# Kernel optimization log

Hardware: AMD Instinct MI355X
Metric: run time of the kernel (lower is better)

## Reference

```python
import jax, jax.numpy as jnp
import numpy as np

N_NODES = 50000
N_EDGES = 1_600_000
IN_DIM = 128
HID = 64


def gcn_conv(x, src, dst, w, W, b, n):
    # PyG GCNConv(normalize=True, add_self_loops=True):
    # add self loops with weight 1, sym-normalize, x@W (no bias in lin), scatter-add, +bias
    loop = jnp.arange(n)
    s = jnp.concatenate([src, loop])
    d = jnp.concatenate([dst, loop])
    ww = jnp.concatenate([w, jnp.ones((n,), w.dtype)])
    deg = jax.ops.segment_sum(ww, d, num_segments=n)                 # [n]
    dis = jnp.where(deg > 0, jax.lax.rsqrt(deg), 0.0)                # deg^{-1/2}, inf->0
    norm = dis[s] * ww * dis[d]                                      # [E+n]
    h = x @ W                                                        # [n, out]
    msg = h[s] * norm[:, None]                                       # gather + scale
    out = jax.ops.segment_sum(msg, d, num_segments=n)                # scatter-add at dst
    return out + b


def setup_inputs() -> dict:
    key = jax.random.key(0)
    ks = jax.random.split(key, 9)
    X = jax.random.normal(ks[0], (N_NODES, IN_DIM), dtype=jnp.float32)
    edge_index = jax.random.randint(ks[1], (2, N_EDGES), 0, N_NODES, dtype=jnp.int64)
    edge_weight = jax.random.uniform(ks[2], (N_EDGES,), dtype=jnp.float32)
    s1 = 1.0 / np.sqrt(IN_DIM)
    s2 = 1.0 / np.sqrt(HID)
    W1 = jax.random.uniform(ks[3], (IN_DIM, HID), jnp.float32, -s1, s1)
    b1 = jax.random.uniform(ks[4], (HID,), jnp.float32, -s1, s1)
    W2 = jax.random.uniform(ks[5], (HID, HID), jnp.float32, -s2, s2)
    b2 = jax.random.uniform(ks[6], (HID,), jnp.float32, -s2, s2)
    Wl = jax.random.uniform(ks[7], (HID, 1), jnp.float32, -s2, s2)
    bl = jax.random.uniform(ks[8], (1,), jnp.float32, -s2, s2)
    return {"X": X, "edge_index": edge_index, "edge_weight": edge_weight,
            "W1": W1, "b1": b1, "W2": W2, "b2": b2, "Wl": Wl, "bl": bl}


def reference(X, edge_index, edge_weight, W1, b1, W2, b2, Wl, bl):
    n = X.shape[0]
    src, dst = edge_index[0], edge_index[1]
    h = jax.nn.relu(gcn_conv(X, src, dst, edge_weight, W1, b1, n))
    # F.dropout(p=0.2) is identity in eval mode
    h = jax.nn.relu(gcn_conv(h, src, dst, edge_weight, W2, b2, n))
    return jax.nn.sigmoid(h @ Wl + bl).squeeze(1)   # [n]
```

## Files before the change

### kernel.cpp

```cpp
#include <hip/hip_runtime.h>

typedef float f32x2 __attribute__((ext_vector_type(2)));

#define A2B 512
#define A2T 512
#define STG 3200

__device__ __forceinline__ long ld_idx(const void* idx, long pos, int is64) {
  return is64 ? (long)((const long long*)idx)[pos]
              : (long)((const int*)idx)[pos];
}

__device__ __forceinline__ int detect_is64(const void* idx) {
  const unsigned long long* p = (const unsigned long long*)idx;
  unsigned long long v = p[threadIdx.x & 63];
  return (__ballot((v >> 32) != 0ull) == 0ull) ? 1 : 0;
}

__global__ __launch_bounds__(256) void k_hist256(const void* __restrict__ idx,
                                                 unsigned* __restrict__ histT,
                                                 long E, int chunk, unsigned M) {
  __shared__ unsigned cnt[256];
  const int b = blockIdx.x, t = threadIdx.x;
  const int is64 = detect_is64(idx);
  cnt[t] = 0;
  __syncthreads();
  const long e0 = (long)b * chunk;
  long e1 = e0 + chunk; if (e1 > E) e1 = E;
  for (long e = e0 + t; e < e1; e += 256) {
    unsigned d = (unsigned)ld_idx(idx, E + e, is64);
    atomicAdd(&cnt[__umulhi(d, M)], 1u);
  }
  __syncthreads();
  histT[(size_t)t * A2B + b] = cnt[t];
}

__global__ __launch_bounds__(256) void k_colscan(const unsigned* __restrict__ histT,
                                                 unsigned* __restrict__ baseT,
                                                 unsigned* __restrict__ colsum) {
  __shared__ unsigned sh[256];
  const int k = blockIdx.x, t = threadIdx.x;
  const uint2 v = ((const uint2*)(histT + (size_t)k * A2B))[t];
  unsigned s = v.x + v.y;
  sh[t] = s;
  __syncthreads();
  for (int off = 1; off < 256; off <<= 1) {
    unsigned u = (t >= off) ? sh[t - off] : 0;
    __syncthreads();
    sh[t] += u;
    __syncthreads();
  }
  unsigned excl = sh[t] - s;
  uint2 o; o.x = excl; o.y = excl + v.x;
  ((uint2*)(baseT + (size_t)k * A2B))[t] = o;
  if (t == 255) colsum[k] = sh[255];
}

__global__ __launch_bounds__(A2T) void k_bucket(const void* __restrict__ idx,
                                                const float* __restrict__ w,
                                                const unsigned* __restrict__ baseT,
                                                const unsigned* __restrict__ colsum,
                                                uint2* __restrict__ recs,
                                                long E, int chunk, unsigned M) {
  __shared__ uint2 stage[STG];
  __shared__ unsigned cnt[256], lofs[256], lbase[256], bcol[256], scanb[256];
  const int b = blockIdx.x, t = threadIdx.x;
  const long e0 = (long)b * chunk;
  long e1 = e0 + chunk; if (e1 > E) e1 = E;
  const int m = (int)(e1 - e0);
  const int is64 = detect_is64(idx);
  if (t < 256) scanb[t] = colsum[t];
  __syncthreads();
  for (int off = 1; off < 256; off <<= 1) {
    unsigned u = 0;
    if (t < 256 && t >= off) u = scanb[t - off];
    __syncthreads();
    if (t < 256) scanb[t] += u;
    __syncthreads();
  }
  if (t < 256) {
    bcol[t] = (scanb[t] - colsum[t]) + baseT[(size_t)t * A2B + b];
    cnt[t] = 0;
  }
  __syncthreads();
  unsigned short dc[8]; unsigned char kc[8];
  int nk = 0;
  for (long e = e0 + t; e < e1; e += A2T, ++nk) {
    unsigned d = (unsigned)ld_idx(idx, E + e, is64);
    unsigned kb = __umulhi(d, M);
    dc[nk] = (unsigned short)d; kc[nk] = (unsigned char)kb;
    atomicAdd(&cnt[kb], 1u);
  }
  __syncthreads();
  if (t < 256) scanb[t] = cnt[t];
  __syncthreads();
  for (int off = 1; off < 256; off <<= 1) {
    unsigned u = 0;
    if (t < 256 && t >= off) u = scanb[t - off];
    __syncthreads();
    if (t < 256) scanb[t] += u;
    __syncthreads();
  }
  if (t < 256) { unsigned ex = scanb[t] - cnt[t]; lbase[t] = ex; lofs[t] = ex; }
  __syncthreads();
  nk = 0;
  for (long e = e0 + t; e < e1; e += A2T, ++nk) {
    unsigned s = (unsigned)ld_idx(idx, e, is64);
    float wv = w[e];
    unsigned kb = kc[nk];
    unsigned pos = atomicAdd(&lofs[kb], 1u);
    stage[pos] = make_uint2(s | ((unsigned)dc[nk] << 16), __float_as_uint(wv));
  }
  __syncthreads();
  for (int i = t; i < m; i += A2T) {
    uint2 r = stage[i];
    unsigned kb = __umulhi(r.x >> 16, M);
    recs[bcol[kb] + (unsigned)i - lbase[kb]] = r;
  }
}

__global__ __launch_bounds__(1024) void k_build(const uint2* __restrict__ recs,
                                                const unsigned* __restrict__ colsum,
                                                int* __restrict__ rowptr,
                                                float* __restrict__ dis,
                                                float2* __restrict__ edges,
                                                int n, int dwidth, long E) {
  __shared__ float wsum[256];
  __shared__ unsigned cnt[256], lofs[256], scanb[256];
  __shared__ int shr0, shr1;
  const int k = blockIdx.x, t = threadIdx.x;
  const int d0 = k * dwidth;
  if (t < 256) scanb[t] = colsum[t];
  __syncthreads();
  for (int off = 1; off < 256; off <<= 1) {
    unsigned u = 0;
    if (t < 256 && t >= off) u = scanb[t - off];
    __syncthreads();
    if (t < 256) scanb[t] += u;
    __syncthreads();
  }
  if (t == k) { shr1 = (int)scanb[t]; shr0 = (int)(scanb[t] - colsum[t]); }
  if (t < 256) { wsum[t] = 0.0f; cnt[t] = 0; }
  __syncthreads();
  const int r0 = shr0, r1 = shr1;
  const int m = r1 - r0;
  for (int i = t; i < m; i += 1024) {
    uint2 r = recs[r0 + i];
    int dl = (int)(r.x >> 16) - d0;
    atomicAdd(&cnt[dl], 1u);
    atomicAdd(&wsum[dl], __uint_as_float(r.y));
  }
  __syncthreads();
  if (t < 256) scanb[t] = cnt[t];
  __syncthreads();
  for (int off = 1; off < 256; off <<= 1) {
    unsigned u = 0;
    if (t < 256 && t >= off) u = scanb[t - off];
    __syncthreads();
    if (t < 256) scanb[t] += u;
    __syncthreads();
  }
  if (t < 256) {
    unsigned ex = scanb[t] - cnt[t];
    lofs[t] = (unsigned)r0 + ex;
    int d = d0 + t;
    if (t < dwidth && d < n) {
      rowptr[d] = r0 + (int)ex;
      dis[d] = rsqrtf(1.0f + wsum[t]);
    }
  }
  if (k == gridDim.x - 1 && t == 0) rowptr[n] = (int)E;
  __syncthreads();
  for (int i = t; i < m; i += 1024) {
    uint2 r = recs[r0 + i];
    unsigned pos = atomicAdd(&lofs[(int)(r.x >> 16) - d0], 1u);
    edges[pos] = make_float2(__uint_as_float(r.x & 0xffffu), __uint_as_float(r.y));
  }
}

__device__ __forceinline__ uint4 pack16_fp8(const float* acc) {
  uint4 o;
  unsigned v;
  v = 0;
  v = __builtin_amdgcn_cvt_pk_fp8_f32(acc[0],  acc[1],  v, false);
  v = __builtin_amdgcn_cvt_pk_fp8_f32(acc[2],  acc[3],  v, true);
  o.x = v; v = 0;
  v = __builtin_amdgcn_cvt_pk_fp8_f32(acc[4],  acc[5],  v, false);
  v = __builtin_amdgcn_cvt_pk_fp8_f32(acc[6],  acc[7],  v, true);
  o.y = v; v = 0;
  v = __builtin_amdgcn_cvt_pk_fp8_f32(acc[8],  acc[9],  v, false);
  v = __builtin_amdgcn_cvt_pk_fp8_f32(acc[10], acc[11], v, true);
  o.z = v; v = 0;
  v = __builtin_amdgcn_cvt_pk_fp8_f32(acc[12], acc[13], v, false);
  v = __builtin_amdgcn_cvt_pk_fp8_f32(acc[14], acc[15], v, true);
  o.w = v;
  return o;
}

__global__ __launch_bounds__(256) void k_gemm1(const float* __restrict__ X,
                                               const float* __restrict__ W,
                                               unsigned char* __restrict__ h, int n) {
  __shared__ float Ws[128 * 64];
  for (int i = threadIdx.x; i < 2048; i += 256)
    ((float4*)Ws)[i] = ((const float4*)W)[i];
  __syncthreads();
  int gid = blockIdx.x * 256 + threadIdx.x;
  int node = gid >> 2;
  int fg = (gid & 3) * 16;
  if (node >= n) return;
  const float4* xr4 = (const float4*)(X + (size_t)node * 128);
  float acc[16];
#pragma unroll
  for (int f = 0; f < 16; ++f) acc[f] = 0.0f;
  for (int k4 = 0; k4 < 32; ++k4) {
    float4 x = xr4[k4];
#pragma unroll
    for (int kk = 0; kk < 4; ++kk) {
      float xv = (kk == 0) ? x.x : (kk == 1) ? x.y : (kk == 2) ? x.z : x.w;
      const float4* wrow = (const float4*)(Ws + (k4 * 4 + kk) * 64 + fg);
#pragma unroll
      for (int f4 = 0; f4 < 4; ++f4) {
        float4 w = wrow[f4];
        acc[f4 * 4 + 0] = fmaf(xv, w.x, acc[f4 * 4 + 0]);
        acc[f4 * 4 + 1] = fmaf(xv, w.y, acc[f4 * 4 + 1]);
        acc[f4 * 4 + 2] = fmaf(xv, w.z, acc[f4 * 4 + 2]);
        acc[f4 * 4 + 3] = fmaf(xv, w.w, acc[f4 * 4 + 3]);
      }
    }
  }
  *(uint4*)(h + (size_t)node * 64 + fg) = pack16_fp8(acc);
}

__global__ __launch_bounds__(256) void k_gemm2(const float* __restrict__ in,
                                               const float* __restrict__ W,
                                               unsigned char* __restrict__ h, int n) {
  __shared__ float Ws[64 * 64];
  for (int i = threadIdx.x; i < 1024; i += 256)
    ((float4*)Ws)[i] = ((const float4*)W)[i];
  __syncthreads();
  int gid = blockIdx.x * 256 + threadIdx.x;
  int node = gid >> 2;
  int fg = (gid & 3) * 16;
  if (node >= n) return;
  const float4* xr4 = (const float4*)(in + (size_t)node * 64);
  float acc[16];
#pragma unroll
  for (int f = 0; f < 16; ++f) acc[f] = 0.0f;
  for (int k4 = 0; k4 < 16; ++k4) {
    float4 x = xr4[k4];
#pragma unroll
    for (int kk = 0; kk < 4; ++kk) {
      float xv = (kk == 0) ? x.x : (kk == 1) ? x.y : (kk == 2) ? x.z : x.w;
      xv = fmaxf(xv, 0.0f);
      const float4* wrow = (const float4*)(Ws + (k4 * 4 + kk) * 64 + fg);
#pragma unroll
      for (int f4 = 0; f4 < 4; ++f4) {
        float4 w = wrow[f4];
        acc[f4 * 4 + 0] = fmaf(xv, w.x, acc[f4 * 4 + 0]);
        acc[f4 * 4 + 1] = fmaf(xv, w.y, acc[f4 * 4 + 1]);
        acc[f4 * 4 + 2] = fmaf(xv, w.z, acc[f4 * 4 + 2]);
        acc[f4 * 4 + 3] = fmaf(xv, w.w, acc[f4 * 4 + 3]);
      }
    }
  }
  *(uint4*)(h + (size_t)node * 64 + fg) = pack16_fp8(acc);
}

template <int MODE>
__global__ __launch_bounds__(256) void k_gather(const unsigned char* __restrict__ h,
                                                const float* __restrict__ dis,
                                                const float2* __restrict__ edges,
                                                const int* __restrict__ rowptr,
                                                const float* __restrict__ b,
                                                const float* __restrict__ Wl,
                                                const float* __restrict__ bl,
                                                float* __restrict__ out, int n) {
  int lane = threadIdx.x & 63;
  int half = lane >> 5;
  int l32 = lane & 31;
  int fl = lane & 7;
  int eg = (lane >> 3) & 3;
  int node = blockIdx.x * 8 + (int)(threadIdx.x >> 6) * 2 + half;
  if (node >= n) return;
  int beg = rowptr[node], end = rowptr[node + 1];
  float s0 = dis[node];
  float acc[8];
#pragma unroll
  for (int i = 0; i < 8; ++i) acc[i] = 0.0f;

  for (int base = beg; base < end; base += 32) {
    int m = end - base; if (m > 32) m = 32;
    float2 pk = (l32 < m) ? edges[base + l32] : make_float2(__int_as_float(0), 0.0f);
    float nrm = dis[__float_as_int(pk.x)] * pk.y * s0;
    int steps = (m + 3) >> 2;
    for (int s = 0; s < steps; ++s) {
      int j = half * 32 + s * 4 + eg;
      int   sj = __float_as_int(__shfl(pk.x, j));
      float nj = __shfl(nrm, j);
      uint2 hv = *(const uint2*)(h + (size_t)sj * 64 + fl * 8);
      f32x2 p0 = __builtin_amdgcn_cvt_pk_f32_fp8(hv.x, false);
      f32x2 p1 = __builtin_amdgcn_cvt_pk_f32_fp8(hv.x, true);
      f32x2 p2 = __builtin_amdgcn_cvt_pk_f32_fp8(hv.y, false);
      f32x2 p3 = __builtin_amdgcn_cvt_pk_f32_fp8(hv.y, true);
      acc[0] = fmaf(p0[0], nj, acc[0]);
      acc[1] = fmaf(p0[1], nj, acc[1]);
      acc[2] = fmaf(p1[0], nj, acc[2]);
      acc[3] = fmaf(p1[1], nj, acc[3]);
      acc[4] = fmaf(p2[0], nj, acc[4]);
      acc[5] = fmaf(p2[1], nj, acc[5]);
      acc[6] = fmaf(p3[0], nj, acc[6]);
      acc[7] = fmaf(p3[1], nj, acc[7]);
    }
  }
#pragma unroll
  for (int off = 8; off < 32; off <<= 1)
#pragma unroll
    for (int i = 0; i < 8; ++i) acc[i] += __shfl_xor(acc[i], off);

  uint2 hv = *(const uint2*)(h + (size_t)node * 64 + fl * 8);
  f32x2 q0 = __builtin_amdgcn_cvt_pk_f32_fp8(hv.x, false);
  f32x2 q1 = __builtin_amdgcn_cvt_pk_f32_fp8(hv.x, true);
  f32x2 q2 = __builtin_amdgcn_cvt_pk_f32_fp8(hv.y, false);
  f32x2 q3 = __builtin_amdgcn_cvt_pk_f32_fp8(hv.y, true);
  float hs[8] = {q0[0], q0[1], q1[0], q1[1], q2[0], q2[1], q3[0], q3[1]};
  float4 bv0 = *(const float4*)(b + fl * 8);
  float4 bv1 = *(const float4*)(b + fl * 8 + 4);
  float bb[8] = {bv0.x, bv0.y, bv0.z, bv0.w, bv1.x, bv1.y, bv1.z, bv1.w};
  float s2 = s0 * s0;
#pragma unroll
  for (int i = 0; i < 8; ++i) acc[i] += bb[i] + hs[i] * s2;

  if (MODE == 0) {
    if (eg == 0) {
      float4 o0 = make_float4(acc[0], acc[1], acc[2], acc[3]);
      float4 o1 = make_float4(acc[4], acc[5], acc[6], acc[7]);
      *(float4*)(out + (size_t)node * 64 + fl * 8) = o0;
      *(float4*)(out + (size_t)node * 64 + fl * 8 + 4) = o1;
    }
  } else {
    float4 wl0 = *(const float4*)(Wl + fl * 8);
    float4 wl1 = *(const float4*)(Wl + fl * 8 + 4);
    float wl[8] = {wl0.x, wl0.y, wl0.z, wl0.w, wl1.x, wl1.y, wl1.z, wl1.w};
    float v = 0.0f;
#pragma unroll
    for (int i = 0; i < 8; ++i) v += fmaxf(acc[i], 0.0f) * wl[i];
#pragma unroll
    for (int off = 1; off < 8; off <<= 1) v += __shfl_xor(v, off);
    if (l32 == 0) out[node] = 1.0f / (1.0f + expf(-(v + bl[0])));
  }
}

extern "C" void kernel_launch(void* const* d_in, const int* in_sizes, int n_in,
                              void* d_out, int out_size, void* d_ws, size_t ws_size,
                              hipStream_t stream) {
  const float* X  = (const float*)d_in[0];
  const void*  EI = d_in[1];
  const float* EW = (const float*)d_in[2];
  const float* W1 = (const float*)d_in[3];
  const float* b1 = (const float*)d_in[4];
  const float* W2 = (const float*)d_in[5];
  const float* b2 = (const float*)d_in[6];
  const float* Wl = (const float*)d_in[7];
  const float* bl = (const float*)d_in[8];
  float* out = (float*)d_out;

  const int  n = in_sizes[0] / 128;
  const long E = (long)in_sizes[1] / 2;

  const int chunk  = (int)((E + A2B - 1) / A2B);
  const int dwidth = (n + 255) / 256;
  const unsigned M = (unsigned)((0x100000000ULL + (unsigned)dwidth - 1) / (unsigned)dwidth);

  auto align = [](size_t x) { return (x + 255) & ~(size_t)255; };
  char* ws = (char*)d_ws;
  size_t off = 0;
  float*         dis    = (float*)(ws + off);         off += align((size_t)n * 4);
  int*           rowptr = (int*)(ws + off);           off += align((size_t)(n + 1) * 4);
  unsigned*      colsum = (unsigned*)(ws + off);      off += align(256 * 4);
  unsigned*      histT  = (unsigned*)(ws + off);      off += align((size_t)A2B * 256 * 4);
  unsigned*      baseT  = (unsigned*)(ws + off);      off += align((size_t)A2B * 256 * 4);
  uint2*         recs   = (uint2*)(ws + off);         off += align((size_t)E * 8);
  float2*        edges  = (float2*)(ws + off);        off += align((size_t)E * 8);
  unsigned char* A      = (unsigned char*)(ws + off); off += align((size_t)n * 64);
  float*         B      = (float*)(ws + off);         off += align((size_t)n * 64 * 4);

  const int nbW = (n + 7) / 8;
  const int nbG = (n * 4 + 255) / 256;

  k_hist256<<<A2B, 256, 0, stream>>>(EI, histT, E, chunk, M);
  k_colscan<<<256, 256, 0, stream>>>(histT, baseT, colsum);
  k_bucket<<<A2B, A2T, 0, stream>>>(EI, EW, baseT, colsum, recs, E, chunk, M);
  k_build<<<256, 1024, 0, stream>>>(recs, colsum, rowptr, dis, edges, n, dwidth, E);

  k_gemm1<<<nbG, dim3(256), 0, stream>>>(X, W1, A, n);
  k_gather<0><<<nbW, dim3(256), 0, stream>>>(A, dis, edges, rowptr, b1, Wl, bl, B, n);

  k_gemm2<<<nbG, dim3(256), 0, stream>>>(B, W2, A, n);
  k_gather<1><<<nbW, dim3(256), 0, stream>>>(A, dis, edges, rowptr, b2, Wl, bl, out, n);
}
```

Measured before the change: 218.8 us.

## Fuse layer-1 aggregation with second GEMM and merge histogram with first GEMM

```diff
diff --git a/kernel.cpp b/kernel.cpp
--- a/kernel.cpp
+++ b/kernel.cpp
@@ -15,167 +15,6 @@
   const unsigned long long* p = (const unsigned long long*)idx;
   unsigned long long v = p[threadIdx.x & 63];
   return (__ballot((v >> 32) != 0ull) == 0ull) ? 1 : 0;
-}
-
-__global__ __launch_bounds__(256) void k_hist256(const void* __restrict__ idx,
-                                                 unsigned* __restrict__ histT,
-                                                 long E, int chunk, unsigned M) {
-  __shared__ unsigned cnt[256];
-  const int b = blockIdx.x, t = threadIdx.x;
-  const int is64 = detect_is64(idx);
-  cnt[t] = 0;
-  __syncthreads();
-  const long e0 = (long)b * chunk;
-  long e1 = e0 + chunk; if (e1 > E) e1 = E;
-  for (long e = e0 + t; e < e1; e += 256) {
-    unsigned d = (unsigned)ld_idx(idx, E + e, is64);
-    atomicAdd(&cnt[__umulhi(d, M)], 1u);
-  }
-  __syncthreads();
-  histT[(size_t)t * A2B + b] = cnt[t];
-}
-
-__global__ __launch_bounds__(256) void k_colscan(const unsigned* __restrict__ histT,
-                                                 unsigned* __restrict__ baseT,
-                                                 unsigned* __restrict__ colsum) {
-  __shared__ unsigned sh[256];
-  const int k = blockIdx.x, t = threadIdx.x;
-  const uint2 v = ((const uint2*)(histT + (size_t)k * A2B))[t];
-  unsigned s = v.x + v.y;
-  sh[t] = s;
-  __syncthreads();
-  for (int off = 1; off < 256; off <<= 1) {
-    unsigned u = (t >= off) ? sh[t - off] : 0;
-    __syncthreads();
-    sh[t] += u;
-    __syncthreads();
-  }
-  unsigned excl = sh[t] - s;
-  uint2 o; o.x = excl; o.y = excl + v.x;
-  ((uint2*)(baseT + (size_t)k * A2B))[t] = o;
-  if (t == 255) colsum[k] = sh[255];
-}
-
-__global__ __launch_bounds__(A2T) void k_bucket(const void* __restrict__ idx,
-                                                const float* __restrict__ w,
-                                                const unsigned* __restrict__ baseT,
-                                                const unsigned* __restrict__ colsum,
-                                                uint2* __restrict__ recs,
-                                                long E, int chunk, unsigned M) {
-  __shared__ uint2 stage[STG];
-  __shared__ unsigned cnt[256], lofs[256], lbase[256], bcol[256], scanb[256];
-  const int b = blockIdx.x, t = threadIdx.x;
-  const long e0 = (long)b * chunk;
-  long e1 = e0 + chunk; if (e1 > E) e1 = E;
-  const int m = (int)(e1 - e0);
-  const int is64 = detect_is64(idx);
-  if (t < 256) scanb[t] = colsum[t];
-  __syncthreads();
-  for (int off = 1; off < 256; off <<= 1) {
-    unsigned u = 0;
-    if (t < 256 && t >= off) u = scanb[t - off];
-    __syncthreads();
-    if (t < 256) scanb[t] += u;
-    __syncthreads();
-  }
-  if (t < 256) {
-    bcol[t] = (scanb[t] - colsum[t]) + baseT[(size_t)t * A2B + b];
-    cnt[t] = 0;
-  }
-  __syncthreads();
-  unsigned short dc[8]; unsigned char kc[8];
-  int nk = 0;
-  for (long e = e0 + t; e < e1; e += A2T, ++nk) {
-    unsigned d = (unsigned)ld_idx(idx, E + e, is64);
-    unsigned kb = __umulhi(d, M);
-    dc[nk] = (unsigned short)d; kc[nk] = (unsigned char)kb;
-    atomicAdd(&cnt[kb], 1u);
-  }
-  __syncthreads();
-  if (t < 256) scanb[t] = cnt[t];
-  __syncthreads();
-  for (int off = 1; off < 256; off <<= 1) {
-    unsigned u = 0;
-    if (t < 256 && t >= off) u = scanb[t - off];
-    __syncthreads();
-    if (t < 256) scanb[t] += u;
-    __syncthreads();
-  }
-  if (t < 256) { unsigned ex = scanb[t] - cnt[t]; lbase[t] = ex; lofs[t] = ex; }
-  __syncthreads();
-  nk = 0;
-  for (long e = e0 + t; e < e1; e += A2T, ++nk) {
-    unsigned s = (unsigned)ld_idx(idx, e, is64);
-    float wv = w[e];
-    unsigned kb = kc[nk];
-    unsigned pos = atomicAdd(&lofs[kb], 1u);
-    stage[pos] = make_uint2(s | ((unsigned)dc[nk] << 16), __float_as_uint(wv));
-  }
-  __syncthreads();
-  for (int i = t; i < m; i += A2T) {
-    uint2 r = stage[i];
-    unsigned kb = __umulhi(r.x >> 16, M);
-    recs[bcol[kb] + (unsigned)i - lbase[kb]] = r;
-  }
-}
-
-__global__ __launch_bounds__(1024) void k_build(const uint2* __restrict__ recs,
-                                                const unsigned* __restrict__ colsum,
-                                                int* __restrict__ rowptr,
-                                                float* __restrict__ dis,
-                                                float2* __restrict__ edges,
-                                                int n, int dwidth, long E) {
-  __shared__ float wsum[256];
-  __shared__ unsigned cnt[256], lofs[256], scanb[256];
-  __shared__ int shr0, shr1;
-  const int k = blockIdx.x, t = threadIdx.x;
-  const int d0 = k * dwidth;
-  if (t < 256) scanb[t] = colsum[t];
-  __syncthreads();
-  for (int off = 1; off < 256; off <<= 1) {
-    unsigned u = 0;
-    if (t < 256 && t >= off) u = scanb[t - off];
-    __syncthreads();
-    if (t < 256) scanb[t] += u;
-    __syncthreads();
-  }
-  if (t == k) { shr1 = (int)scanb[t]; shr0 = (int)(scanb[t] - colsum[t]); }
-  if (t < 256) { wsum[t] = 0.0f; cnt[t] = 0; }
-  __syncthreads();
-  const int r0 = shr0, r1 = shr1;
-  const int m = r1 - r0;
-  for (int i = t; i < m; i += 1024) {
-    uint2 r = recs[r0 + i];
-    int dl = (int)(r.x >> 16) - d0;
-    atomicAdd(&cnt[dl], 1u);
-    atomicAdd(&wsum[dl], __uint_as_float(r.y));
-  }
-  __syncthreads();
-  if (t < 256) scanb[t] = cnt[t];
-  __syncthreads();
-  for (int off = 1; off < 256; off <<= 1) {
-    unsigned u = 0;
-    if (t < 256 && t >= off) u = scanb[t - off];
-    __syncthreads();
-    if (t < 256) scanb[t] += u;
-    __syncthreads();
-  }
-  if (t < 256) {
-    unsigned ex = scanb[t] - cnt[t];
-    lofs[t] = (unsigned)r0 + ex;
-    int d = d0 + t;
-    if (t < dwidth && d < n) {
-      rowptr[d] = r0 + (int)ex;
-      dis[d] = rsqrtf(1.0f + wsum[t]);
-    }
-  }
-  if (k == gridDim.x - 1 && t == 0) rowptr[n] = (int)E;
-  __syncthreads();
-  for (int i = t; i < m; i += 1024) {
-    uint2 r = recs[r0 + i];
-    unsigned pos = atomicAdd(&lofs[(int)(r.x >> 16) - d0], 1u);
-    edges[pos] = make_float2(__uint_as_float(r.x & 0xffffu), __uint_as_float(r.y));
-  }
 }
 
 __device__ __forceinline__ uint4 pack16_fp8(const float* acc) {
@@ -197,14 +36,35 @@
   return o;
 }
 
-__global__ __launch_bounds__(256) void k_gemm1(const float* __restrict__ X,
-                                               const float* __restrict__ W,
+__global__ __launch_bounds__(256) void k_front(const void* __restrict__ idx,
+                                               unsigned* __restrict__ histT,
+                                               long E, int chunk, unsigned M,
+                                               const float* __restrict__ X,
+                                               const float* __restrict__ W1,
                                                unsigned char* __restrict__ h, int n) {
-  __shared__ float Ws[128 * 64];
-  for (int i = threadIdx.x; i < 2048; i += 256)
-    ((float4*)Ws)[i] = ((const float4*)W)[i];
-  __syncthreads();
-  int gid = blockIdx.x * 256 + threadIdx.x;
+  __shared__ float smem[2048];
+  const int t = threadIdx.x;
+  if (blockIdx.x < A2B) {
+    unsigned* cnt = (unsigned*)smem;
+    const int b = blockIdx.x;
+    const int is64 = detect_is64(idx);
+    cnt[t] = 0;
+    __syncthreads();
+    const long e0 = (long)b * chunk;
+    long e1 = e0 + chunk; if (e1 > E) e1 = E;
+    for (long e = e0 + t; e < e1; e += 256) {
+      unsigned d = (unsigned)ld_idx(idx, E + e, is64);
+      atomicAdd(&cnt[__umulhi(d, M)], 1u);
+    }
+    __syncthreads();
+    histT[(size_t)t * A2B + b] = cnt[t];
+    return;
+  }
+  float* Ws = smem;
+  for (int i = t; i < 2048; i += 256)
+    ((float4*)Ws)[i] = ((const float4*)W1)[i];
+  __syncthreads();
+  int gid = (blockIdx.x - A2B) * 256 + t;
   int node = gid >> 2;
   int fg = (gid & 3) * 16;
   if (node >= n) return;
@@ -231,63 +91,157 @@
   *(uint4*)(h + (size_t)node * 64 + fg) = pack16_fp8(acc);
 }
 
-__global__ __launch_bounds__(256) void k_gemm2(const float* __restrict__ in,
-                                               const float* __restrict__ W,
-                                               unsigned char* __restrict__ h, int n) {
-  __shared__ float Ws[64 * 64];
-  for (int i = threadIdx.x; i < 1024; i += 256)
-    ((float4*)Ws)[i] = ((const float4*)W)[i];
-  __syncthreads();
-  int gid = blockIdx.x * 256 + threadIdx.x;
-  int node = gid >> 2;
-  int fg = (gid & 3) * 16;
-  if (node >= n) return;
-  const float4* xr4 = (const float4*)(in + (size_t)node * 64);
-  float acc[16];
-#pragma unroll
-  for (int f = 0; f < 16; ++f) acc[f] = 0.0f;
-  for (int k4 = 0; k4 < 16; ++k4) {
-    float4 x = xr4[k4];
-#pragma unroll
-    for (int kk = 0; kk < 4; ++kk) {
-      float xv = (kk == 0) ? x.x : (kk == 1) ? x.y : (kk == 2) ? x.z : x.w;
-      xv = fmaxf(xv, 0.0f);
-      const float4* wrow = (const float4*)(Ws + (k4 * 4 + kk) * 64 + fg);
-#pragma unroll
-      for (int f4 = 0; f4 < 4; ++f4) {
-        float4 w = wrow[f4];
-        acc[f4 * 4 + 0] = fmaf(xv, w.x, acc[f4 * 4 + 0]);
-        acc[f4 * 4 + 1] = fmaf(xv, w.y, acc[f4 * 4 + 1]);
-        acc[f4 * 4 + 2] = fmaf(xv, w.z, acc[f4 * 4 + 2]);
-        acc[f4 * 4 + 3] = fmaf(xv, w.w, acc[f4 * 4 + 3]);
-      }
+__global__ __launch_bounds__(256) void k_colscan(const unsigned* __restrict__ histT,
+                                                 unsigned* __restrict__ baseT,
+                                                 unsigned* __restrict__ colsum) {
+  __shared__ unsigned sh[256];
+  const int k = blockIdx.x, t = threadIdx.x;
+  const uint2 v = ((const uint2*)(histT + (size_t)k * A2B))[t];
+  unsigned s = v.x + v.y;
+  sh[t] = s;
+  __syncthreads();
+  for (int off = 1; off < 256; off <<= 1) {
+    unsigned u = (t >= off) ? sh[t - off] : 0;
+    __syncthreads();
+    sh[t] += u;
+    __syncthreads();
+  }
+  unsigned excl = sh[t] - s;
+  uint2 o; o.x = excl; o.y = excl + v.x;
+  ((uint2*)(baseT + (size_t)k * A2B))[t] = o;
+  if (t == 255) colsum[k] = sh[255];
+}
+
+__global__ __launch_bounds__(A2T) void k_bucket(const void* __restrict__ idx,
+                                                const float* __restrict__ w,
+                                                const unsigned* __restrict__ baseT,
+                                                const unsigned* __restrict__ colsum,
+                                                uint2* __restrict__ recs,
+                                                long E, int chunk, unsigned M) {
+  __shared__ uint2 stage[STG];
+  __shared__ unsigned cnt[256], lofs[256], lbase[256], bcol[256], scanb[256];
+  const int b = blockIdx.x, t = threadIdx.x;
+  const long e0 = (long)b * chunk;
+  long e1 = e0 + chunk; if (e1 > E) e1 = E;
+  const int m = (int)(e1 - e0);
+  const int is64 = detect_is64(idx);
+  if (t < 256) scanb[t] = colsum[t];
+  __syncthreads();
+  for (int off = 1; off < 256; off <<= 1) {
+    unsigned u = 0;
+    if (t < 256 && t >= off) u = scanb[t - off];
+    __syncthreads();
+    if (t < 256) scanb[t] += u;
+    __syncthreads();
+  }
+  if (t < 256) {
+    bcol[t] = (scanb[t] - colsum[t]) + baseT[(size_t)t * A2B + b];
+    cnt[t] = 0;
+  }
+  __syncthreads();
+  unsigned short dc[8]; unsigned char kc[8];
+  int nk = 0;
+  for (long e = e0 + t; e < e1; e += A2T, ++nk) {
+    unsigned d = (unsigned)ld_idx(idx, E + e, is64);
+    unsigned kb = __umulhi(d, M);
+    dc[nk] = (unsigned short)d; kc[nk] = (unsigned char)kb;
+    atomicAdd(&cnt[kb], 1u);
+  }
+  __syncthreads();
+  if (t < 256) scanb[t] = cnt[t];
+  __syncthreads();
+  for (int off = 1; off < 256; off <<= 1) {
+    unsigned u = 0;
+    if (t < 256 && t >= off) u = scanb[t - off];
+    __syncthreads();
+    if (t < 256) scanb[t] += u;
+    __syncthreads();
+  }
+  if (t < 256) { unsigned ex = scanb[t] - cnt[t]; lbase[t] = ex; lofs[t] = ex; }
+  __syncthreads();
+  nk = 0;
+  for (long e = e0 + t; e < e1; e += A2T, ++nk) {
+    unsigned s = (unsigned)ld_idx(idx, e, is64);
+    float wv = w[e];
+    unsigned kb = kc[nk];
+    unsigned pos = atomicAdd(&lofs[kb], 1u);
+    stage[pos] = make_uint2(s | ((unsigned)dc[nk] << 16), __float_as_uint(wv));
+  }
+  __syncthreads();
+  for (int i = t; i < m; i += A2T) {
+    uint2 r = stage[i];
+    unsigned kb = __umulhi(r.x >> 16, M);
+    recs[bcol[kb] + (unsigned)i - lbase[kb]] = r;
+  }
+}
+
+__global__ __launch_bounds__(1024) void k_build(const uint2* __restrict__ recs,
+                                                const unsigned* __restrict__ colsum,
+                                                int* __restrict__ rowptr,
+                                                float* __restrict__ dis,
+                                                float2* __restrict__ edges,
+                                                int n, int dwidth, long E) {
+  __shared__ float wsum[256];
+  __shared__ unsigned cnt[256], lofs[256], scanb[256];
+  __shared__ int shr0, shr1;
+  const int k = blockIdx.x, t = threadIdx.x;
+  const int d0 = k * dwidth;
+  if (t < 256) scanb[t] = colsum[t];
+  __syncthreads();
+  for (int off = 1; off < 256; off <<= 1) {
+    unsigned u = 0;
+    if (t < 256 && t >= off) u = scanb[t - off];
+    __syncthreads();
+    if (t < 256) scanb[t] += u;
+    __syncthreads();
+  }
+  if (t == k) { shr1 = (int)scanb[t]; shr0 = (int)(scanb[t] - colsum[t]); }
+  if (t < 256) { wsum[t] = 0.0f; cnt[t] = 0; }
+  __syncthreads();
+  const int r0 = shr0, r1 = shr1;
+  const int m = r1 - r0;
+  for (int i = t; i < m; i += 1024) {
+    uint2 r = recs[r0 + i];
+    int dl = (int)(r.x >> 16) - d0;
+    atomicAdd(&cnt[dl], 1u);
+    atomicAdd(&wsum[dl], __uint_as_float(r.y));
+  }
+  __syncthreads();
+  if (t < 256) scanb[t] = cnt[t];
+  __syncthreads();
+  for (int off = 1; off < 256; off <<= 1) {
+    unsigned u = 0;
+    if (t < 256 && t >= off) u = scanb[t - off];
+    __syncthreads();
+    if (t < 256) scanb[t] += u;
+    __syncthreads();
+  }
+  if (t < 256) {
+    unsigned ex = scanb[t] - cnt[t];
+    lofs[t] = (unsigned)r0 + ex;
+    int d = d0 + t;
+    if (t < dwidth && d < n) {
+      rowptr[d] = r0 + (int)ex;
+      dis[d] = rsqrtf(1.0f + wsum[t]);
     }
   }
-  *(uint4*)(h + (size_t)node * 64 + fg) = pack16_fp8(acc);
-}
-
-template <int MODE>
-__global__ __launch_bounds__(256) void k_gather(const unsigned char* __restrict__ h,
-                                                const float* __restrict__ dis,
-                                                const float2* __restrict__ edges,
-                                                const int* __restrict__ rowptr,
-                                                const float* __restrict__ b,
-                                                const float* __restrict__ Wl,
-                                                const float* __restrict__ bl,
-                                                float* __restrict__ out, int n) {
-  int lane = threadIdx.x & 63;
-  int half = lane >> 5;
-  int l32 = lane & 31;
-  int fl = lane & 7;
-  int eg = (lane >> 3) & 3;
-  int node = blockIdx.x * 8 + (int)(threadIdx.x >> 6) * 2 + half;
-  if (node >= n) return;
-  int beg = rowptr[node], end = rowptr[node + 1];
-  float s0 = dis[node];
-  float acc[8];
+  if (k == gridDim.x - 1 && t == 0) rowptr[n] = (int)E;
+  __syncthreads();
+  for (int i = t; i < m; i += 1024) {
+    uint2 r = recs[r0 + i];
+    unsigned pos = atomicAdd(&lofs[(int)(r.x >> 16) - d0], 1u);
+    edges[pos] = make_float2(__uint_as_float(r.x & 0xffffu), __uint_as_float(r.y));
+  }
+}
+
+__device__ __forceinline__ void gather_acc(const unsigned char* __restrict__ h,
+                                           const float* __restrict__ dis,
+                                           const float2* __restrict__ edges,
+                                           int beg, int end, float s0,
+                                           int half, int l32, int fl, int eg,
+                                           float* acc) {
 #pragma unroll
   for (int i = 0; i < 8; ++i) acc[i] = 0.0f;
-
   for (int base = beg; base < end; base += 32) {
     int m = end - base; if (m > 32) m = 32;
     float2 pk = (l32 < m) ? edges[base + l32] : make_float2(__int_as_float(0), 0.0f);
@@ -316,7 +270,11 @@
   for (int off = 8; off < 32; off <<= 1)
 #pragma unroll
     for (int i = 0; i < 8; ++i) acc[i] += __shfl_xor(acc[i], off);
-
+}
+
+__device__ __forceinline__ void add_bias_self(const unsigned char* __restrict__ h,
+                                              const float* __restrict__ b,
+                                              int node, int fl, float s0, float* acc) {
   uint2 hv = *(const uint2*)(h + (size_t)node * 64 + fl * 8);
   f32x2 q0 = __builtin_amdgcn_cvt_pk_f32_fp8(hv.x, false);
   f32x2 q1 = __builtin_amdgcn_cvt_pk_f32_fp8(hv.x, true);
@@ -329,25 +287,85 @@
   float s2 = s0 * s0;
 #pragma unroll
   for (int i = 0; i < 8; ++i) acc[i] += bb[i] + hs[i] * s2;
-
-  if (MODE == 0) {
+}
+
+__global__ __launch_bounds__(256) void k_gather_mid(const unsigned char* __restrict__ h,
+                                                    const float* __restrict__ dis,
+                                                    const float2* __restrict__ edges,
+                                                    const int* __restrict__ rowptr,
+                                                    const float* __restrict__ b1,
+                                                    const float* __restrict__ W2,
+                                                    unsigned char* __restrict__ h2, int n) {
+  __shared__ float W2s[64 * 64];
+  __shared__ float xs[8 * 64];
+  const int t = threadIdx.x;
+  for (int i = t; i < 1024; i += 256)
+    ((float4*)W2s)[i] = ((const float4*)W2)[i];
+  int lane = t & 63;
+  int half = lane >> 5;
+  int l32 = lane & 31;
+  int fl = lane & 7;
+  int eg = (lane >> 3) & 3;
+  int nl = t >> 5;
+  int node = blockIdx.x * 8 + nl;
+  int beg = 0, end = 0; float s0 = 0.0f;
+  if (node < n) { beg = rowptr[node]; end = rowptr[node + 1]; s0 = dis[node]; }
+  float acc[8];
+  gather_acc(h, dis, edges, beg, end, s0, half, l32, fl, eg, acc);
+  if (node < n) {
+    add_bias_self(h, b1, node, fl, s0, acc);
     if (eg == 0) {
-      float4 o0 = make_float4(acc[0], acc[1], acc[2], acc[3]);
-      float4 o1 = make_float4(acc[4], acc[5], acc[6], acc[7]);
-      *(float4*)(out + (size_t)node * 64 + fl * 8) = o0;
-      *(float4*)(out + (size_t)node * 64 + fl * 8 + 4) = o1;
+#pragma unroll
+      for (int i = 0; i < 8; ++i) xs[nl * 64 + fl * 8 + i] = fmaxf(acc[i], 0.0f);
     }
-  } else {
-    float4 wl0 = *(const float4*)(Wl + fl * 8);
-    float4 wl1 = *(const float4*)(Wl + fl * 8 + 4);
-    float wl[8] = {wl0.x, wl0.y, wl0.z, wl0.w, wl1.x, wl1.y, wl1.z, wl1.w};
-    float v = 0.0f;
-#pragma unroll
-    for (int i = 0; i < 8; ++i) v += fmaxf(acc[i], 0.0f) * wl[i];
-#pragma unroll
-    for (int off = 1; off < 8; off <<= 1) v += __shfl_xor(v, off);
-    if (l32 == 0) out[node] = 1.0f / (1.0f + expf(-(v + bl[0])));
-  }
+  }
+  __syncthreads();
+  int tl = l32;
+  int node2 = blockIdx.x * 8 + (t >> 5);
+  if (node2 >= n) return;
+  const float* xrow = xs + (t >> 5) * 64;
+  int f = tl * 2;
+  float a0 = 0.0f, a1 = 0.0f;
+#pragma unroll 8
+  for (int k = 0; k < 64; ++k) {
+    float xk = xrow[k];
+    f32x2 wv = *(const f32x2*)(W2s + k * 64 + f);
+    a0 = fmaf(xk, wv[0], a0);
+    a1 = fmaf(xk, wv[1], a1);
+  }
+  unsigned v = __builtin_amdgcn_cvt_pk_fp8_f32(a0, a1, 0u, false);
+  *(unsigned short*)(h2 + (size_t)node2 * 64 + f) = (unsigned short)v;
+}
+
+__global__ __launch_bounds__(256) void k_gather_fin(const unsigned char* __restrict__ h,
+                                                    const float* __restrict__ dis,
+                                                    const float2* __restrict__ edges,
+                                                    const int* __restrict__ rowptr,
+                                                    const float* __restrict__ b2,
+                                                    const float* __restrict__ Wl,
+                                                    const float* __restrict__ bl,
+                                                    float* __restrict__ out, int n) {
+  int lane = threadIdx.x & 63;
+  int half = lane >> 5;
+  int l32 = lane & 31;
+  int fl = lane & 7;
+  int eg = (lane >> 3) & 3;
+  int node = blockIdx.x * 8 + (int)(threadIdx.x >> 5);
+  if (node >= n) return;
+  int beg = rowptr[node], end = rowptr[node + 1];
+  float s0 = dis[node];
+  float acc[8];
+  gather_acc(h, dis, edges, beg, end, s0, half, l32, fl, eg, acc);
+  add_bias_self(h, b2, node, fl, s0, acc);
+  float4 wl0 = *(const float4*)(Wl + fl * 8);
+  float4 wl1 = *(const float4*)(Wl + fl * 8 + 4);
+  float wl[8] = {wl0.x, wl0.y, wl0.z, wl0.w, wl1.x, wl1.y, wl1.z, wl1.w};
+  float v = 0.0f;
+#pragma unroll
+  for (int i = 0; i < 8; ++i) v += fmaxf(acc[i], 0.0f) * wl[i];
+#pragma unroll
+  for (int off = 1; off < 8; off <<= 1) v += __shfl_xor(v, off);
+  if (l32 == 0) out[node] = 1.0f / (1.0f + expf(-(v + bl[0])));
 }
 
 extern "C" void kernel_launch(void* const* d_in, const int* in_sizes, int n_in,
@@ -382,19 +400,16 @@
   uint2*         recs   = (uint2*)(ws + off);         off += align((size_t)E * 8);
   float2*        edges  = (float2*)(ws + off);        off += align((size_t)E * 8);
   unsigned char* A      = (unsigned char*)(ws + off); off += align((size_t)n * 64);
-  float*         B      = (float*)(ws + off);         off += align((size_t)n * 64 * 4);
+  unsigned char* A2     = (unsigned char*)(ws + off); off += align((size_t)n * 64);
 
   const int nbW = (n + 7) / 8;
   const int nbG = (n * 4 + 255) / 256;
 
-  k_hist256<<<A2B, 256, 0, stream>>>(EI, histT, E, chunk, M);
+  k_front<<<A2B + nbG, dim3(256), 0, stream>>>(EI, histT, E, chunk, M, X, W1, A, n);
   k_colscan<<<256, 256, 0, stream>>>(histT, baseT, colsum);
   k_bucket<<<A2B, A2T, 0, stream>>>(EI, EW, baseT, colsum, recs, E, chunk, M);
   k_build<<<256, 1024, 0, stream>>>(recs, colsum, rowptr, dis, edges, n, dwidth, E);
 
-  k_gemm1<<<nbG, dim3(256), 0, stream>>>(X, W1, A, n);
-  k_gather<0><<<nbW, dim3(256), 0, stream>>>(A, dis, edges, rowptr, b1, Wl, bl, B, n);
-
-  k_gemm2<<<nbG, dim3(256), 0, stream>>>(B, W2, A, n);
-  k_gather<1><<<nbW, dim3(256), 0, stream>>>(A, dis, edges, rowptr, b2, Wl, bl, out, n);
-}
+  k_gather_mid<<<nbW, dim3(256), 0, stream>>>(A, dis, edges, rowptr, b1, W2, A2, n);
+  k_gather_fin<<<nbW, dim3(256), 0, stream>>>(A2, dis, edges, rowptr, b2, Wl, bl, out, n);
+}
```

Result: faster. 211.7 us (-3.2%).
